# Performance work log

Hardware: AMD Instinct MI355X
Metric: run time of the kernel (lower is better)

Reference implementation:

```python
import jax, jax.numpy as jnp
import numpy as np

K = 4            # number of modes (init kwarg)
ALPHA = 2000.0   # bandwidth constraint
TAU = 0.0        # dual ascent step (0 -> exact reconstruction slack)
N_ITERS = 20     # fixed ADMM iterations (orig: tol-based while loop, max 500)


def vmd_batch(x):
    # x: [B, C, T] float32 -> (u: [B, C, K, T], omega: [B, C, K])
    B, C, T = x.shape
    T2 = 2 * T
    half = T2 // 2
    # mirror extension (vmdpy): flip first half | signal | flip second half
    f = jnp.concatenate([x[..., :T // 2][..., ::-1], x, x[..., T // 2:][..., ::-1]], axis=-1)  # [B,C,T2]
    t = jnp.arange(1, T2 + 1, dtype=jnp.float32) / T2
    freqs = t - 0.5 - 1.0 / T2                       # [T2], centered frequency axis
    freqs_pos = freqs[half:]                          # [T], positive frequencies
    f_hat = jnp.fft.fftshift(jnp.fft.fft(f, axis=-1), axes=-1).astype(jnp.complex64)
    f_hat_plus = f_hat.at[..., :half].set(0.0)        # keep analytic (positive-freq) part
    # init=1: uniform initial center frequencies
    omega = jnp.broadcast_to((0.5 / K) * jnp.arange(K, dtype=jnp.float32), (B, C, K))
    u_hat = jnp.zeros((B, C, K, T2), dtype=jnp.complex64)
    lam = jnp.zeros((B, C, T2), dtype=jnp.complex64)  # dual variable lambda_hat

    def step(carry, _):
        u_hat, omega, lam = carry
        S = jnp.sum(u_hat, axis=2)                    # running sum of all modes [B,C,T2]
        new_u, new_w = [], []
        for k in range(K):                            # Gauss-Seidel sweep over K modes (K small, unrolled)
            S = S - u_hat[:, :, k]                    # sum of all other modes (updated ones included)
            denom = 1.0 + ALPHA * (freqs[None, None, :] - omega[:, :, k:k + 1]) ** 2
            uk = (f_hat_plus - S + lam / 2.0) / denom # Wiener-filter spectral update [B,C,T2]
            S = S + uk
            p = uk.real[..., half:] ** 2 + uk.imag[..., half:] ** 2  # power on positive freqs [B,C,T]
            wk = jnp.sum(freqs_pos * p, axis=-1) / jnp.sum(p, axis=-1)  # center-frequency re-estimate
            new_u.append(uk)
            new_w.append(wk)
        u_hat = jnp.stack(new_u, axis=2)
        omega = jnp.stack(new_w, axis=-1)
        lam = lam + TAU * (S - f_hat_plus)            # dual ascent (tau=0 -> no-op, kept for fidelity)
        return (u_hat, omega, lam), None

    (u_hat, omega, lam), _ = jax.lax.scan(step, (u_hat, omega, lam), None, length=N_ITERS)

    # reconstruct full conjugate-symmetric spectrum
    pos = u_hat[..., half:]                           # [B,C,K,T]
    full = jnp.zeros((B, C, K, T2), dtype=jnp.complex64)
    full = full.at[..., half:].set(pos)
    full = full.at[..., 1:half + 1].set(jnp.conj(pos)[..., ::-1])  # full[half-j] = conj(pos[j])
    full = full.at[..., 0].set(jnp.conj(full[..., -1]))
    u = jnp.real(jnp.fft.ifft(jnp.fft.ifftshift(full, axes=-1), axis=-1))  # [B,C,K,T2]
    u = u[..., T2 // 4: 3 * T2 // 4]                  # de-mirror: center T samples
    return u, omega


def setup_inputs() -> dict:
    key = jax.random.key(0)
    x = jax.random.normal(key, (16, 8192, 4), dtype=jnp.float32)  # [B, T, C]
    return {"x": x}


def reference(x):
    # module forward: permute [B,T,C] -> [B,C,T], run VMD, return u:[B,K,T,C], omega:[B,K]
    u, omega = vmd_batch(jnp.transpose(x, (0, 2, 1)))
    u = jnp.transpose(u, (0, 2, 3, 1))                # [B,K,T,C]
    omega_b = jnp.mean(omega, axis=1)                 # collapse channel dim -> [B,K]
    return (u, omega_b)
```

## Files before the change

### kernel.cpp

```cpp
#include <hip/hip_runtime.h>


#define HALF      8192
#define NH        8192
#define NTHREADS  1024
#define KMODES    4
#define NITERS    20
#define ALPHA_F   2000.0f
#define SQH       0.70710678118654752440f
#define SENTINEL  0xFFFFFFFFu

typedef __fp16 half2_t __attribute__((ext_vector_type(2)));
typedef float  v2f     __attribute__((ext_vector_type(2)));

__device__ __forceinline__ unsigned bitrev13(unsigned x) { return __brev(x) >> 19; }
__device__ __forceinline__ int pidx(int i) { return i + (i >> 4); }

__device__ __forceinline__ unsigned pack_h2(float a, float b) {
    half2_t h = __builtin_amdgcn_cvt_pkrtz(a, b);
    return __builtin_bit_cast(unsigned, h);
}
__device__ __forceinline__ v2f unpack_h2(unsigned u) {
    half2_t h = __builtin_bit_cast(half2_t, u);
    v2f r; r.x = (float)h.x; r.y = (float)h.y; return r;
}

__device__ __forceinline__ unsigned ic_load(const unsigned* p) {
    return __hip_atomic_load(p, __ATOMIC_RELAXED, __HIP_MEMORY_SCOPE_AGENT);
}
__device__ __forceinline__ void ic_store(unsigned* p, unsigned v) {
    __hip_atomic_store(p, v, __ATOMIC_RELAXED, __HIP_MEMORY_SCOPE_AGENT);
}

template <int CTRL>
__device__ __forceinline__ float dpp_add_step(float v) {
    int r = __builtin_amdgcn_update_dpp(0, __float_as_int(v), CTRL, 0xf, 0xf, true);
    return v + __int_as_float(r);
}
__device__ __forceinline__ float wave64_sum(float v) {
    v = dpp_add_step<0x111>(v);
    v = dpp_add_step<0x112>(v);
    v = dpp_add_step<0x114>(v);
    v = dpp_add_step<0x118>(v);
    v = dpp_add_step<0x142>(v);
    v = dpp_add_step<0x143>(v);
    return v;
}

__device__ __forceinline__ float2 cmul(float2 a, float wr, float wi) {
    return make_float2(a.x * wr - a.y * wi, a.x * wi + a.y * wr);
}
__device__ __forceinline__ float2 cadd(float2 a, float2 b) {
    return make_float2(a.x + b.x, a.y + b.y);
}
__device__ __forceinline__ float2 csub(float2 a, float2 b) {
    return make_float2(a.x - b.x, a.y - b.y);
}

template <bool INV>
__device__ __forceinline__ void fft_pass8(float2* A, int tid, int t) {
    const int   log2Q = 10 - 3 * t;
    const int   Q     = 1 << log2Q;
    const float invL  = (float)(1 << (3 * t)) * (1.0f / 8192.0f);
    const int j    = tid & (Q - 1);
    const int base = ((tid >> log2Q) << (log2Q + 3)) + j;

    float2 x[8];
    #pragma unroll
    for (int m = 0; m < 8; ++m) x[m] = A[pidx(base + m * Q)];

    float rev = (float)j * invL;
    float w1r = __builtin_amdgcn_cosf(rev);
    float w1i = INV ?  __builtin_amdgcn_sinf(rev)
                    : -__builtin_amdgcn_sinf(rev);
    float w2r = w1r * w1r - w1i * w1i, w2i = 2.0f * w1r * w1i;
    float w4r = w2r * w2r - w2i * w2i, w4i = 2.0f * w2r * w2i;
    float wsr, wsi;
    if (INV) { wsr = SQH * (w1r - w1i); wsi = SQH * (w1r + w1i); }
    else     { wsr = SQH * (w1r + w1i); wsi = SQH * (w1i - w1r); }
    float w1tr = INV ? -w1i : w1i,  w1ti = INV ? w1r : -w1r;
    float wstr = INV ? -wsi : wsi,  wsti = INV ? wsr : -wsr;
    float w2tr = INV ? -w2i : w2i,  w2ti = INV ? w2r : -w2r;

    float2 y0 = cadd(x[0], x[4]), y1 = cadd(x[1], x[5]);
    float2 y2 = cadd(x[2], x[6]), y3 = cadd(x[3], x[7]);
    float2 y4 = cmul(csub(x[0], x[4]), w1r, w1i);
    float2 y5 = cmul(csub(x[1], x[5]), wsr, wsi);
    float2 y6 = cmul(csub(x[2], x[6]), w1tr, w1ti);
    float2 y7 = cmul(csub(x[3], x[7]), wstr, wsti);

    float2 z0 = cadd(y0, y2), z2 = cmul(csub(y0, y2), w2r, w2i);
    float2 z1 = cadd(y1, y3), z3 = cmul(csub(y1, y3), w2tr, w2ti);
    float2 z4 = cadd(y4, y6), z6 = cmul(csub(y4, y6), w2r, w2i);
    float2 z5 = cadd(y5, y7), z7 = cmul(csub(y5, y7), w2tr, w2ti);

    A[pidx(base + 0 * Q)] = cadd(z0, z1);
    A[pidx(base + 1 * Q)] = cmul(csub(z0, z1), w4r, w4i);
    A[pidx(base + 2 * Q)] = cadd(z2, z3);
    A[pidx(base + 3 * Q)] = cmul(csub(z2, z3), w4r, w4i);
    A[pidx(base + 4 * Q)] = cadd(z4, z5);
    A[pidx(base + 5 * Q)] = cmul(csub(z4, z5), w4r, w4i);
    A[pidx(base + 6 * Q)] = cadd(z6, z7);
    A[pidx(base + 7 * Q)] = cmul(csub(z6, z7), w4r, w4i);
}

__device__ __forceinline__ void fft_last2(float2* A, int tid) {
    #pragma unroll
    for (int u = 0; u < 4; ++u) {
        int t  = tid + u * NTHREADS;
        int i0 = 2 * t, i1 = 2 * t + 1;
        float2 a = A[pidx(i0)], b = A[pidx(i1)];
        A[pidx(i0)] = make_float2(a.x + b.x, a.y + b.y);
        A[pidx(i1)] = make_float2(a.x - b.x, a.y - b.y);
    }
}

__device__ __forceinline__ int mirror_t(int i) {
    if (i < 4096)       return 4095 - i;
    else if (i < 12288) return i - 4096;
    else                return 20479 - i;
}

__global__ __launch_bounds__(NTHREADS) void vmd_fused(
    const float* __restrict__ x, unsigned* __restrict__ ws_u,
    unsigned* __restrict__ ws_omega, unsigned* __restrict__ ws_part,
    unsigned* __restrict__ ws_udone, float* __restrict__ out)
{
    __shared__ float2 A[NH + (NH >> 4)];
    const int tid = threadIdx.x;
    const int bid = blockIdx.x;
    const int ch  = bid & 63;
    const int q   = bid >> 6;
    const int b   = ch >> 2, c = ch & 3;
    const float* xb = x + (size_t)b * 8192 * 4 + c;

    for (int m = tid; m < NH; m += NTHREADS) {
        float re = xb[(size_t)mirror_t(2 * m) * 4];
        float im = xb[(size_t)mirror_t(2 * m + 1) * 4];
        A[pidx(m)] = make_float2(re, im);
    }
    __syncthreads();

    for (int t = 0; t < 4; ++t) {
        fft_pass8<false>(A, tid, t);
        __syncthreads();
    }
    fft_last2(A, tid);
    __syncthreads();

    v2f R[2];
    #pragma unroll
    for (int u = 0; u < 2; ++u) {
        int j  = (q << 11) + tid + u * NTHREADS;
        float2 z1 = A[pidx((int)bitrev13((unsigned)j))];
        float2 z2 = A[pidx((int)bitrev13((unsigned)((NH - j) & (NH - 1))))];
        float ex = 0.5f * (z1.x + z2.x);
        float ey = 0.5f * (z1.y - z2.y);
        float dx = 0.5f * (z1.x - z2.x);
        float dy = 0.5f * (z1.y + z2.y);
        float rev = (float)j * (1.0f / 16384.0f);
        float wr = __builtin_amdgcn_cosf(rev);
        float wi = -__builtin_amdgcn_sinf(rev);
        R[u].x = ex + wr * dy + wi * dx;
        R[u].y = ey + wi * dy - wr * dx;
    }
    __syncthreads();

    v2f Up[KMODES][2];
    #pragma unroll
    for (int u = 0; u < 2; ++u)
        #pragma unroll
        for (int k = 0; k < KMODES; ++k) { Up[k][u].x = 0.f; Up[k][u].y = 0.f; }

    const float f0 = (float)((q << 11) + tid) * (1.0f / 16384.0f);
    float omg[KMODES] = {0.0f, 0.125f, 0.25f, 0.375f};

    float* red = (float*)A;
    const int lane = tid & 63, wid = tid >> 6;

    for (int it = 0; it < NITERS; ++it) {
        v2f nd[KMODES];
        #pragma unroll
        for (int k = 0; k < KMODES; ++k) { nd[k].x = 0.f; nd[k].y = 0.f; }
        #pragma unroll
        for (int u = 0; u < 2; ++u) {
            const float fru = f0 + (float)u * 0.0625f;
            v2f fv; fv.x = fru; fv.y = 1.0f;
            #pragma unroll
            for (int k = 0; k < KMODES; ++k) {
                float d   = fru - omg[k];
                float dnm = fmaf(ALPHA_F * d, d, 1.0f);
                float rcp = __builtin_amdgcn_rcpf(dnm);
                v2f uo  = Up[k][u];
                v2f nm  = R[u] + uo;
                v2f un  = nm * rcp;
                R[u]    = nm - un;
                Up[k][u] = un;
                float p = fmaf(un.x, un.x, un.y * un.y);
                nd[k]   = fv * p + nd[k];
            }
        }
        float num[KMODES], den[KMODES];
        #pragma unroll
        for (int m = 0; m < KMODES; ++m) {
            num[m] = wave64_sum(nd[m].x);
            den[m] = wave64_sum(nd[m].y);
        }
        float* redb = red + (it & 1) * 144;
        if (lane == 63) {
            float4* r4 = (float4*)&redb[wid * 8];
            r4[0] = make_float4(num[0], num[1], num[2], num[3]);
            r4[1] = make_float4(den[0], den[1], den[2], den[3]);
        }
        __syncthreads();
        const bool last_it = (it == NITERS - 1);
        unsigned* pp = ws_part + (((size_t)it * 64 + ch) << 5);
        if (wid == 0) {
            float v = redb[lane] + redb[lane + 64];
            v += __int_as_float(__builtin_amdgcn_ds_swizzle(__float_as_int(v), 0x201F));
            v += __int_as_float(__builtin_amdgcn_ds_swizzle(__float_as_int(v), 0x401F));
            v += __int_as_float(__builtin_amdgcn_ds_bpermute((lane ^ 32) << 2,
                                                             __float_as_int(v)));
            if (lane < 8)
                ic_store(pp + (q << 3) + lane, __float_as_uint(v));
            if (!last_it || q == 0) {
                float t = 0.0f;
                if (lane < 32) {
                    unsigned w;
                    for (;;) {
                        w = ic_load(pp + lane);
                        if (w != SENTINEL) break;
                        __builtin_amdgcn_s_sleep(1);
                    }
                    t = __uint_as_float(w);
                }
                t += __int_as_float(__builtin_amdgcn_ds_swizzle(__float_as_int(t), 0x201F));
                t += __int_as_float(__builtin_amdgcn_ds_swizzle(__float_as_int(t), 0x401F));
                if (!last_it) {
                    if (lane < 8) redb[128 + lane] = t;
                } else {
                    #pragma unroll
                    for (int m = 0; m < KMODES; ++m) {
                        float nm_ = __int_as_float(__builtin_amdgcn_readlane(__float_as_int(t), m));
                        float dn_ = __int_as_float(__builtin_amdgcn_readlane(__float_as_int(t), m + 4));
                        omg[m] = nm_ * __builtin_amdgcn_rcpf(dn_);
                    }
                }
            }
        }
        if (!last_it) {
            __syncthreads();
            #pragma unroll
            for (int m = 0; m < KMODES; ++m) {
                float nm_ = redb[128 + m];
                float dn_ = redb[128 + m + 4];
                omg[m] = nm_ * __builtin_amdgcn_rcpf(dn_);
            }
        }
    }

    #pragma unroll
    for (int k = 0; k < KMODES; ++k) {
        unsigned* dst = ws_u + (size_t)(ch * KMODES + k) * HALF + (q << 11);
        #pragma unroll
        for (int u = 0; u < 2; ++u)
            ic_store(dst + tid + u * NTHREADS, pack_h2(Up[k][u].x, Up[k][u].y));
    }
    if (q == 0 && tid < KMODES)
        ic_store(ws_omega + ch * KMODES + tid, __float_as_uint(omg[tid]));
    asm volatile("s_waitcnt vmcnt(0)" ::: "memory");
    __syncthreads();
    if (tid == 0)
        ic_store(ws_udone + (ch << 2) + q, 0u);

    const int g2  = bid & 63;
    const int c2  = bid >> 6;
    const int b2  = g2 >> 2, k2 = g2 & 3;
    const int ch2 = b2 * 4 + c2;
    const unsigned* pos = ws_u + (size_t)(ch2 * KMODES + k2) * HALF;

    if (bid == 0 && tid < 64) {
        int bb = tid >> 2, kk = tid & 3;
        float s = 0.f;
        #pragma unroll
        for (int cc = 0; cc < 4; ++cc) {
            const unsigned* p = ws_omega + ((bb * 4 + cc) << 2) + kk;
            unsigned w;
            for (;;) {
                w = ic_load(p);
                if (w != SENTINEL) break;
                __builtin_amdgcn_s_sleep(1);
            }
            s += __uint_as_float(w);
        }
        out[2097152 + tid] = 0.25f * s;
    }

    if (tid < 4) {
        const unsigned* p = ws_udone + (ch2 << 2) + tid;
        for (;;) {
            unsigned w = ic_load(p);
            if (w != SENTINEL) break;
            __builtin_amdgcn_s_sleep(1);
        }
    }
    __syncthreads();

    {
        unsigned wj[8], wh[8];
        #pragma unroll
        for (int uu = 0; uu < 8; ++uu) {
            int j = tid + uu * NTHREADS;
            wj[uu] = ic_load(pos + j);
            wh[uu] = ic_load(pos + (j ? (HALF - j) : (HALF - 1)));
        }
        #pragma unroll
        for (int uu = 0; uu < 8; ++uu) {
            int j = tid + uu * NTHREADS;
            v2f pj = unpack_h2(wj[uu]);
            v2f ph = unpack_h2(wh[uu]);
            float gjx = pj.x, gjy = (j == 0) ? -pj.y : pj.y;
            float ghx = ph.x, ghy = -ph.y;
            float ex = 0.5f * (gjx + ghx), ey = 0.5f * (gjy + ghy);
            float dx = 0.5f * (gjx - ghx), dy = 0.5f * (gjy - ghy);
            float rev = (float)j * (1.0f / 16384.0f);
            float wr = __builtin_amdgcn_cosf(rev);
            float wi = __builtin_amdgcn_sinf(rev);
            float ox = dx * wr - dy * wi;
            float oy = dx * wi + dy * wr;
            A[pidx(j)] = make_float2(ex - oy, ey + ox);
        }
    }
    __syncthreads();

    for (int t = 0; t < 4; ++t) {
        fft_pass8<true>(A, tid, t);
        __syncthreads();
    }
    fft_last2(A, tid);
    __syncthreads();

    float* outp = out + (size_t)(b2 * 4 + k2) * 8192 * 4 + c2;
    for (int m = 2048 + tid; m < 6144; m += NTHREADS) {
        float2 z = A[pidx((int)bitrev13((unsigned)m))];
        int t0 = 2 * m - 4096;
        outp[(size_t)t0 * 4]       = z.x * (1.0f / 8192.0f);
        outp[(size_t)(t0 + 1) * 4] = z.y * (1.0f / 8192.0f);
    }
}

extern "C" void kernel_launch(void* const* d_in, const int* in_sizes, int n_in,
                              void* d_out, int out_size, void* d_ws, size_t ws_size,
                              hipStream_t stream)
{
    (void)in_sizes; (void)n_in; (void)out_size; (void)ws_size;
    const float* x = (const float*)d_in[0];
    float* out = (float*)d_out;

    unsigned* ws_u     = (unsigned*)d_ws;
    unsigned* ws_omega = (unsigned*)((char*)d_ws + (size_t)64 * 4 * HALF * 4);
    unsigned* ws_part  = ws_omega + 256;
    unsigned* ws_udone = ws_part + (size_t)NITERS * 64 * 32;

    hipMemsetAsync(ws_omega, 0xFF,
                   (size_t)(256 + NITERS * 64 * 32 + 256) * 4, stream);
    vmd_fused<<<256, NTHREADS, 0, stream>>>(x, ws_u, ws_omega, ws_part,
                                            ws_udone, out);
}
```

Before: 84.61 us.

## Remap blocks so channel quarters share an XCD and add fast-path partial exchange

Block-to-channel mapping is changed so the four quarter-blocks of a channel are likely scheduled on the same XCD, assuming round-robin dispatch across 8 XCDs. The per-iteration partial sums are now written twice: a plain store that is read with sc0 (local L2 coherence), plus an agent-scope atomic copy as a fallback. The aim is to cut the latency of the per-iteration inter-block reduction spin-wait. It relies on the hardware dispatch order to be fast, keeps the slow path for correctness, and doubles the memset workspace.

```diff
diff --git a/kernel.cpp b/kernel.cpp
--- a/kernel.cpp
+++ b/kernel.cpp
@@ -30,6 +30,16 @@
 }
 __device__ __forceinline__ void ic_store(unsigned* p, unsigned v) {
     __hip_atomic_store(p, v, __ATOMIC_RELAXED, __HIP_MEMORY_SCOPE_AGENT);
+}
+__device__ __forceinline__ void store_plain(unsigned* p, unsigned v) {
+    asm volatile("global_store_dword %0, %1, off" :: "v"(p), "v"(v) : "memory");
+}
+__device__ __forceinline__ unsigned load_sc0(const unsigned* p) {
+    unsigned r;
+    asm volatile("global_load_dword %0, %1, off sc0\n\t"
+                 "s_waitcnt vmcnt(0)"
+                 : "=v"(r) : "v"(p) : "memory");
+    return r;
 }
 
 template <int CTRL>
@@ -123,14 +133,17 @@
 
 __global__ __launch_bounds__(NTHREADS) void vmd_fused(
     const float* __restrict__ x, unsigned* __restrict__ ws_u,
-    unsigned* __restrict__ ws_omega, unsigned* __restrict__ ws_part,
-    unsigned* __restrict__ ws_udone, float* __restrict__ out)
+    unsigned* __restrict__ ws_omega, unsigned* __restrict__ ws_partf,
+    unsigned* __restrict__ ws_parts, unsigned* __restrict__ ws_udone,
+    float* __restrict__ out)
 {
     __shared__ float2 A[NH + (NH >> 4)];
     const int tid = threadIdx.x;
     const int bid = blockIdx.x;
-    const int ch  = bid & 63;
-    const int q   = bid >> 6;
+    const int r8  = bid & 7;
+    const int q   = (bid >> 3) & 3;
+    const int a8  = bid >> 5;
+    const int ch  = a8 * 8 + r8;
     const int b   = ch >> 2, c = ch & 3;
     const float* xb = x + (size_t)b * 8192 * 4 + c;
 
@@ -214,21 +227,27 @@
         }
         __syncthreads();
         const bool last_it = (it == NITERS - 1);
-        unsigned* pp = ws_part + (((size_t)it * 64 + ch) << 5);
+        unsigned* ppf = ws_partf + (((size_t)it * 64 + ch) << 5);
+        unsigned* pps = ws_parts + (((size_t)it * 64 + ch) << 5);
         if (wid == 0) {
             float v = redb[lane] + redb[lane + 64];
             v += __int_as_float(__builtin_amdgcn_ds_swizzle(__float_as_int(v), 0x201F));
             v += __int_as_float(__builtin_amdgcn_ds_swizzle(__float_as_int(v), 0x401F));
             v += __int_as_float(__builtin_amdgcn_ds_bpermute((lane ^ 32) << 2,
                                                              __float_as_int(v)));
-            if (lane < 8)
-                ic_store(pp + (q << 3) + lane, __float_as_uint(v));
+            if (lane < 8) {
+                unsigned bits = __float_as_uint(v);
+                store_plain(ppf + (q << 3) + lane, bits);
+                ic_store(pps + (q << 3) + lane, bits);
+            }
             if (!last_it || q == 0) {
                 float t = 0.0f;
                 if (lane < 32) {
                     unsigned w;
                     for (;;) {
-                        w = ic_load(pp + lane);
+                        w = load_sc0(ppf + lane);
+                        if (w != SENTINEL) break;
+                        w = ic_load(pps + lane);
                         if (w != SENTINEL) break;
                         __builtin_amdgcn_s_sleep(1);
                     }
@@ -359,11 +378,12 @@
 
     unsigned* ws_u     = (unsigned*)d_ws;
     unsigned* ws_omega = (unsigned*)((char*)d_ws + (size_t)64 * 4 * HALF * 4);
-    unsigned* ws_part  = ws_omega + 256;
-    unsigned* ws_udone = ws_part + (size_t)NITERS * 64 * 32;
+    unsigned* ws_partf = ws_omega + 256;
+    unsigned* ws_parts = ws_partf + (size_t)NITERS * 64 * 32;
+    unsigned* ws_udone = ws_parts + (size_t)NITERS * 64 * 32;
 
     hipMemsetAsync(ws_omega, 0xFF,
-                   (size_t)(256 + NITERS * 64 * 32 + 256) * 4, stream);
-    vmd_fused<<<256, NTHREADS, 0, stream>>>(x, ws_u, ws_omega, ws_part,
-                                            ws_udone, out);
-}
+                   (size_t)(256 + 2 * NITERS * 64 * 32 + 256) * 4, stream);
+    vmd_fused<<<256, NTHREADS, 0, stream>>>(x, ws_u, ws_omega, ws_partf,
+                                            ws_parts, ws_udone, out);
+}
```

Result: no change. 83.46 us (-1.4%).
